# Performance work log

Measured on AMD Instinct MI355X. Metric: run time of the kernel, lower is better.

Reference implementation:

```python
import jax, jax.numpy as jnp
import numpy as np

E4M3_MAX = 448.0
E5M2_MAX = 57344.0

def _q(t, scale, max_rep, dt):
    # divide by scale, saturate to representable range, cast to fp8 (matches torch .to(float8) saturation)
    return jnp.clip(t.astype(jnp.float32) / scale, -max_rep, max_rep).astype(dt)

def setup_inputs() -> dict:
    key = jax.random.key(0)
    k1, k2, k3 = jax.random.split(key, 3)
    B, S, K, N = 4, 2048, 4096, 16384
    x = jax.random.normal(k1, (B, S, K), dtype=jnp.float32).astype(jnp.bfloat16)
    weight = (jax.random.normal(k2, (N, K), dtype=jnp.float32) * 0.02).astype(jnp.bfloat16)
    bias = (jax.random.normal(k3, (N,), dtype=jnp.float32) * 0.01).astype(jnp.bfloat16)
    return {
        "x": x,
        "weight": weight,
        "bias": bias,
        "x_scale": jnp.ones((1,), jnp.float32),   # cold-start unit scales, as in the module
        "w_scale": jnp.ones((1,), jnp.float32),
        "gy_scale": jnp.ones((1,), jnp.float32),
    }

def reference(x, weight, bias, x_scale, w_scale, gy_scale):
    # y = dequant(q_e4m3(x/sx)) @ dequant(q_e4m3(W/sw)).T + b, accumulated in fp32, emitted bf16
    N, K = weight.shape
    leading = x.shape[:-1]
    x_flat = x.reshape(-1, K)                                  # [M, K]
    x_q = _q(x_flat, x_scale, E4M3_MAX, jnp.float8_e4m3fn)     # E4M3 activations
    w_q = _q(weight, w_scale, E4M3_MAX, jnp.float8_e4m3fn)     # E4M3 weights
    x_deq = x_q.astype(jnp.float32) * x_scale                  # cuBLASLt applies scale_a*scale_b in epilogue
    w_deq = w_q.astype(jnp.float32) * w_scale
    y = jnp.einsum('mk,nk->mn', x_deq, w_deq) + bias.astype(jnp.float32)
    return y.astype(jnp.bfloat16).reshape(*leading, N)
```

## Files before the change

### kernel.cpp

```cpp
#include <hip/hip_runtime.h>
#include <hip/hip_bf16.h>
#include <stdint.h>

typedef float f32x4 __attribute__((ext_vector_type(4)));
typedef float f32x16 __attribute__((ext_vector_type(16)));
typedef int i32x4 __attribute__((ext_vector_type(4)));
typedef int i32x8 __attribute__((ext_vector_type(8)));
typedef long i64;

#define BM 256
#define BN 128
#define BKB 64

__device__ __host__ __forceinline__ int swz(int r) {
  return ((r >> 1) ^ (r >> 3)) & 3;
}

__global__ __launch_bounds__(256) void quant_fp8_from_f32(
    const float* __restrict__ in, const float* __restrict__ scale,
    uint8_t* __restrict__ out, int n16) {
  const int i = blockIdx.x * blockDim.x + threadIdx.x;
  if (i >= n16) return;
  const float inv_s = 1.0f / scale[0];
  const float* p = in + (i64)i * 16;
  f32x4 v[4];
  v[0] = *(const f32x4*)p;
  v[1] = *(const f32x4*)(p + 4);
  v[2] = *(const f32x4*)(p + 8);
  v[3] = *(const f32x4*)(p + 12);
  uint32_t w[4];
#pragma unroll
  for (int q = 0; q < 4; q++) {
    float f0 = fminf(fmaxf(v[q][0] * inv_s, -448.f), 448.f);
    float f1 = fminf(fmaxf(v[q][1] * inv_s, -448.f), 448.f);
    float f2 = fminf(fmaxf(v[q][2] * inv_s, -448.f), 448.f);
    float f3 = fminf(fmaxf(v[q][3] * inv_s, -448.f), 448.f);
    int r = 0;
    r = __builtin_amdgcn_cvt_pk_fp8_f32(f0, f1, r, false);
    r = __builtin_amdgcn_cvt_pk_fp8_f32(f2, f3, r, true);
    w[q] = (uint32_t)r;
  }
  ((uint4*)out)[i] = make_uint4(w[0], w[1], w[2], w[3]);
}

__device__ __forceinline__ void gload_lds16(const void* g, void* l) {
  __builtin_amdgcn_global_load_lds(
      (const __attribute__((address_space(1))) uint32_t*)g,
      (__attribute__((address_space(3))) uint32_t*)l, 16, 0, 0);
}

__device__ __forceinline__ float bf16_rne_f32(float f) {
  union { float f; uint32_t u; } c; c.f = f;
  uint32_t lsb = (c.u >> 16) & 1u;
  c.u += 0x7FFFu + lsb;
  c.u &= 0xFFFF0000u;
  return c.f;
}

__global__ __launch_bounds__(256, 2) void gemm_fp8_mx(
    const uint8_t* __restrict__ Aq, const uint8_t* __restrict__ Bq,
    const float* __restrict__ bias,
    const float* __restrict__ xs, const float* __restrict__ wsc,
    float* __restrict__ C, int M, int N, int K) {
  __shared__ uint8_t sA[2][BM * BKB];
  __shared__ uint8_t sB[2][BN * BKB];

  const int nbn = N / BN;
  int bid = blockIdx.x;
  { int cpx = gridDim.x >> 3; bid = (bid & 7) * cpx + (bid >> 3); }
  const int bm = bid / nbn;
  const int bn = bid % nbn;

  const int t = threadIdx.x, lane = t & 63, wave = t >> 6;
  const int wm = (wave >> 1) * 128;
  const int wn = (wave & 1) * 64;
  const int g = lane >> 5;
  const int r31 = lane & 31;

  f32x16 acc[4][2];
#pragma unroll
  for (int i = 0; i < 4; i++)
#pragma unroll
    for (int j = 0; j < 2; j++) acc[i][j] = (f32x16)0.f;

  const int srow = t >> 2;
  const int c16 = t & 3;
  i64 src[4];
#pragma unroll
  for (int j = 0; j < 4; j++) {
    const int row = srow + 64 * j;
    src[j] = (i64)row * K + ((c16 ^ swz(row)) << 4);
  }
  const uint8_t* gA = Aq + (i64)(bm * BM) * K;
  const uint8_t* gB = Bq + (i64)(bn * BN) * K;

  int aoff[4][2], boff[2][2];
#pragma unroll
  for (int i = 0; i < 4; i++) {
    const int ra = wm + i * 32 + r31;
    const int sa_ = swz(ra);
    aoff[i][0] = ra * 64 + (((2 * g + 0) ^ sa_) << 4);
    aoff[i][1] = ra * 64 + (((2 * g + 1) ^ sa_) << 4);
  }
#pragma unroll
  for (int j = 0; j < 2; j++) {
    const int rb = wn + j * 32 + r31;
    const int sb_ = swz(rb);
    boff[j][0] = rb * 64 + (((2 * g + 0) ^ sb_) << 4);
    boff[j][1] = rb * 64 + (((2 * g + 1) ^ sb_) << 4);
  }

  const int NT = K / BKB;
#pragma unroll
  for (int j = 0; j < 4; j++)
    gload_lds16(gA + src[j], &sA[0][t * 16 + j * 4096]);
#pragma unroll
  for (int j = 0; j < 2; j++)
    gload_lds16(gB + src[j], &sB[0][t * 16 + j * 4096]);

  int cur = 0;
  for (int it = 0; it < NT; ++it) {
    if (it + 1 < NT) {
      const i64 kt = (i64)(it + 1) * BKB;
      const int nxt = cur ^ 1;
#pragma unroll
      for (int j = 0; j < 4; j++)
        gload_lds16(gA + src[j] + kt, &sA[nxt][t * 16 + j * 4096]);
#pragma unroll
      for (int j = 0; j < 2; j++)
        gload_lds16(gB + src[j] + kt, &sB[nxt][t * 16 + j * 4096]);
      asm volatile("s_waitcnt vmcnt(6)" ::: "memory");
    } else {
      asm volatile("s_waitcnt vmcnt(0)" ::: "memory");
    }
    __builtin_amdgcn_s_barrier();

    union opnd { i32x4 h[2]; i32x8 v; };
    union opnd ub[2];
#pragma unroll
    for (int j = 0; j < 2; j++) {
      ub[j].h[0] = *(const i32x4*)(&sB[cur][0] + boff[j][0]);
      ub[j].h[1] = *(const i32x4*)(&sB[cur][0] + boff[j][1]);
    }
#pragma unroll
    for (int i = 0; i < 4; i++) {
      union opnd ua;
      ua.h[0] = *(const i32x4*)(&sA[cur][0] + aoff[i][0]);
      ua.h[1] = *(const i32x4*)(&sA[cur][0] + aoff[i][1]);
#pragma unroll
      for (int j = 0; j < 2; j++)
        acc[i][j] = __builtin_amdgcn_mfma_scale_f32_32x32x64_f8f6f4(
            ua.v, ub[j].v, acc[i][j],
            0, 0,
            0, 127,
            0, 127);
    }

    __builtin_amdgcn_s_barrier();
    cur ^= 1;
  }

  const float sc = xs[0] * wsc[0];
#pragma unroll
  for (int j = 0; j < 2; j++) {
    const int col = bn * BN + wn + j * 32 + r31;
    const float bv = bias[col];
#pragma unroll
    for (int i = 0; i < 4; i++) {
      const int rowbase = bm * BM + wm + i * 32 + 4 * g;
#pragma unroll
      for (int reg = 0; reg < 16; reg++) {
        const int row = rowbase + (reg & 3) + 8 * (reg >> 2);
        C[(i64)row * N + col] = bf16_rne_f32(acc[i][j][reg] * sc + bv);
      }
    }
  }
}

extern "C" void kernel_launch(void* const* d_in, const int* in_sizes, int n_in,
                              void* d_out, int out_size, void* d_ws, size_t ws_size,
                              hipStream_t stream) {
  const float* x = (const float*)d_in[0];
  const float* w = (const float*)d_in[1];
  const float* bias = (const float*)d_in[2];
  const float* x_scale = (const float*)d_in[3];
  const float* w_scale = (const float*)d_in[4];

  const int N = in_sizes[2];
  const int K = in_sizes[1] / N;
  const int M = in_sizes[0] / K;

  uint8_t* xq = (uint8_t*)d_ws;
  uint8_t* wq = (uint8_t*)d_ws + (size_t)M * K;

  {
    const int n16 = (M * K) / 16;
    quant_fp8_from_f32<<<(n16 + 255) / 256, 256, 0, stream>>>(x, x_scale, xq, n16);
  }
  {
    const int n16 = (int)(((i64)N * K) / 16);
    quant_fp8_from_f32<<<(n16 + 255) / 256, 256, 0, stream>>>(w, w_scale, wq, n16);
  }

  dim3 grid((M / BM) * (N / BN));
  gemm_fp8_mx<<<grid, 256, 0, stream>>>(
      xq, wq, bias, x_scale, w_scale, (float*)d_out, M, N, K);
}
```

Measured before the change: 723.4 us.

## Load B operand directly from global into registers, bypassing LDS

The weight (B) tile is no longer staged through shared memory. Each wave now loads its own B fragments from global memory straight into registers, one K-step ahead, using ping-pong register buffers, and the loop is unrolled by two to alternate them. The aim is to cut LDS traffic and LDS footprint and to remove the B ds_reads. In exchange, waves that share columns both read the same B data from global memory, the per-row 32-byte accesses coalesce less well, register pressure rises, and the code assumes an even number of K tiles.

```diff
diff --git a/kernel.cpp b/kernel.cpp
--- a/kernel.cpp
+++ b/kernel.cpp
@@ -63,7 +63,6 @@
     const float* __restrict__ xs, const float* __restrict__ wsc,
     float* __restrict__ C, int M, int N, int K) {
   __shared__ uint8_t sA[2][BM * BKB];
-  __shared__ uint8_t sB[2][BN * BKB];
 
   const int nbn = N / BN;
   int bid = blockIdx.x;
@@ -92,9 +91,13 @@
     src[j] = (i64)row * K + ((c16 ^ swz(row)) << 4);
   }
   const uint8_t* gA = Aq + (i64)(bm * BM) * K;
-  const uint8_t* gB = Bq + (i64)(bn * BN) * K;
-
-  int aoff[4][2], boff[2][2];
+
+  const uint8_t* bbase[2];
+#pragma unroll
+  for (int j = 0; j < 2; j++)
+    bbase[j] = Bq + (i64)(bn * BN + wn + j * 32 + r31) * K + g * 32;
+
+  int aoff[4][2];
 #pragma unroll
   for (int i = 0; i < 4; i++) {
     const int ra = wm + i * 32 + r31;
@@ -102,63 +105,56 @@
     aoff[i][0] = ra * 64 + (((2 * g + 0) ^ sa_) << 4);
     aoff[i][1] = ra * 64 + (((2 * g + 1) ^ sa_) << 4);
   }
-#pragma unroll
-  for (int j = 0; j < 2; j++) {
-    const int rb = wn + j * 32 + r31;
-    const int sb_ = swz(rb);
-    boff[j][0] = rb * 64 + (((2 * g + 0) ^ sb_) << 4);
-    boff[j][1] = rb * 64 + (((2 * g + 1) ^ sb_) << 4);
-  }
 
   const int NT = K / BKB;
+  union opnd { i32x4 h[2]; i32x8 v; };
+  opnd ubA[2], ubB[2];
+
 #pragma unroll
   for (int j = 0; j < 4; j++)
     gload_lds16(gA + src[j], &sA[0][t * 16 + j * 4096]);
 #pragma unroll
-  for (int j = 0; j < 2; j++)
-    gload_lds16(gB + src[j], &sB[0][t * 16 + j * 4096]);
-
-  int cur = 0;
-  for (int it = 0; it < NT; ++it) {
-    if (it + 1 < NT) {
-      const i64 kt = (i64)(it + 1) * BKB;
-      const int nxt = cur ^ 1;
-#pragma unroll
-      for (int j = 0; j < 4; j++)
-        gload_lds16(gA + src[j] + kt, &sA[nxt][t * 16 + j * 4096]);
-#pragma unroll
-      for (int j = 0; j < 2; j++)
-        gload_lds16(gB + src[j] + kt, &sB[nxt][t * 16 + j * 4096]);
-      asm volatile("s_waitcnt vmcnt(6)" ::: "memory");
-    } else {
-      asm volatile("s_waitcnt vmcnt(0)" ::: "memory");
-    }
-    __builtin_amdgcn_s_barrier();
-
-    union opnd { i32x4 h[2]; i32x8 v; };
-    union opnd ub[2];
-#pragma unroll
-    for (int j = 0; j < 2; j++) {
-      ub[j].h[0] = *(const i32x4*)(&sB[cur][0] + boff[j][0]);
-      ub[j].h[1] = *(const i32x4*)(&sB[cur][0] + boff[j][1]);
-    }
-#pragma unroll
-    for (int i = 0; i < 4; i++) {
-      union opnd ua;
-      ua.h[0] = *(const i32x4*)(&sA[cur][0] + aoff[i][0]);
-      ua.h[1] = *(const i32x4*)(&sA[cur][0] + aoff[i][1]);
-#pragma unroll
-      for (int j = 0; j < 2; j++)
-        acc[i][j] = __builtin_amdgcn_mfma_scale_f32_32x32x64_f8f6f4(
-            ua.v, ub[j].v, acc[i][j],
-            0, 0,
-            0, 127,
-            0, 127);
-    }
-
-    __builtin_amdgcn_s_barrier();
-    cur ^= 1;
-  }
+  for (int j = 0; j < 2; j++) {
+    ubA[j].h[0] = *(const i32x4*)(bbase[j] + 0);
+    ubA[j].h[1] = *(const i32x4*)(bbase[j] + 16);
+  }
+
+#define STEP(PARITY, UBC, UBN, ITV)                                          \
+  {                                                                          \
+    const int itv = (ITV);                                                   \
+    if (itv + 1 < NT) {                                                      \
+      const i64 kt = (i64)(itv + 1) * BKB;                                   \
+      _Pragma("unroll")                                                      \
+      for (int j = 0; j < 4; j++)                                            \
+        gload_lds16(gA + src[j] + kt, &sA[PARITY ^ 1][t * 16 + j * 4096]);   \
+      _Pragma("unroll")                                                      \
+      for (int j = 0; j < 2; j++) {                                          \
+        UBN[j].h[0] = *(const i32x4*)(bbase[j] + kt);                        \
+        UBN[j].h[1] = *(const i32x4*)(bbase[j] + kt + 16);                   \
+      }                                                                      \
+      asm volatile("s_waitcnt vmcnt(8)" ::: "memory");                       \
+    } else {                                                                 \
+      asm volatile("s_waitcnt vmcnt(0)" ::: "memory");                       \
+    }                                                                        \
+    __builtin_amdgcn_s_barrier();                                            \
+    _Pragma("unroll")                                                        \
+    for (int i = 0; i < 4; i++) {                                            \
+      opnd ua;                                                               \
+      ua.h[0] = *(const i32x4*)(&sA[PARITY][0] + aoff[i][0]);                \
+      ua.h[1] = *(const i32x4*)(&sA[PARITY][0] + aoff[i][1]);                \
+      _Pragma("unroll")                                                      \
+      for (int j = 0; j < 2; j++)                                            \
+        acc[i][j] = __builtin_amdgcn_mfma_scale_f32_32x32x64_f8f6f4(         \
+            ua.v, UBC[j].v, acc[i][j], 0, 0, 0, 127, 0, 127);                \
+    }                                                                        \
+    __builtin_amdgcn_s_barrier();                                            \
+  }
+
+  for (int it = 0; it < NT; it += 2) {
+    STEP(0, ubA, ubB, it);
+    STEP(1, ubB, ubA, it + 1);
+  }
+#undef STEP
 
   const float sc = xs[0] * wsc[0];
 #pragma unroll
```

After: 814.1 us. +12.5%, slower.

## Triple-buffer LDS tiles with prefetch distance two and drop trailing barrier

Applied to the files above, without the earlier changes.

The shared-memory pipeline for the FP8 GEMM goes from two buffers to three. Global-to-LDS loads are now issued two K-tiles ahead, after the B operands for the current tile have been read into registers. With a third buffer, the barrier at the end of each iteration can be removed, since the buffer being overwritten was last read one iteration earlier, before the single remaining barrier. Wave priority is raised around the MFMA block to favour math issue. The cost is 72 KB of LDS per block instead of 48 KB, which tightens occupancy headroom.

```diff
diff --git a/kernel.cpp b/kernel.cpp
--- a/kernel.cpp
+++ b/kernel.cpp
@@ -62,8 +62,8 @@
     const float* __restrict__ bias,
     const float* __restrict__ xs, const float* __restrict__ wsc,
     float* __restrict__ C, int M, int N, int K) {
-  __shared__ uint8_t sA[2][BM * BKB];
-  __shared__ uint8_t sB[2][BN * BKB];
+  __shared__ uint8_t sA[3][BM * BKB];
+  __shared__ uint8_t sB[3][BN * BKB];
 
   const int nbn = N / BN;
   int bid = blockIdx.x;
@@ -112,41 +112,55 @@
 
   const int NT = K / BKB;
 #pragma unroll
-  for (int j = 0; j < 4; j++)
+  for (int j = 0; j < 4; j++) {
     gload_lds16(gA + src[j], &sA[0][t * 16 + j * 4096]);
+  }
 #pragma unroll
   for (int j = 0; j < 2; j++)
     gload_lds16(gB + src[j], &sB[0][t * 16 + j * 4096]);
-
-  int cur = 0;
+#pragma unroll
+  for (int j = 0; j < 4; j++)
+    gload_lds16(gA + src[j] + BKB, &sA[1][t * 16 + j * 4096]);
+#pragma unroll
+  for (int j = 0; j < 2; j++)
+    gload_lds16(gB + src[j] + BKB, &sB[1][t * 16 + j * 4096]);
+
+  int cur = 0, st2 = 2;
   for (int it = 0; it < NT; ++it) {
     if (it + 1 < NT) {
-      const i64 kt = (i64)(it + 1) * BKB;
-      const int nxt = cur ^ 1;
-#pragma unroll
-      for (int j = 0; j < 4; j++)
-        gload_lds16(gA + src[j] + kt, &sA[nxt][t * 16 + j * 4096]);
-#pragma unroll
-      for (int j = 0; j < 2; j++)
-        gload_lds16(gB + src[j] + kt, &sB[nxt][t * 16 + j * 4096]);
       asm volatile("s_waitcnt vmcnt(6)" ::: "memory");
     } else {
       asm volatile("s_waitcnt vmcnt(0)" ::: "memory");
     }
     __builtin_amdgcn_s_barrier();
 
+    const uint8_t* bufA = &sA[cur][0];
+    const uint8_t* bufB = &sB[cur][0];
+
     union opnd { i32x4 h[2]; i32x8 v; };
-    union opnd ub[2];
+    opnd ub[2];
 #pragma unroll
     for (int j = 0; j < 2; j++) {
-      ub[j].h[0] = *(const i32x4*)(&sB[cur][0] + boff[j][0]);
-      ub[j].h[1] = *(const i32x4*)(&sB[cur][0] + boff[j][1]);
-    }
+      ub[j].h[0] = *(const i32x4*)(bufB + boff[j][0]);
+      ub[j].h[1] = *(const i32x4*)(bufB + boff[j][1]);
+    }
+
+    if (it + 2 < NT) {
+      const i64 kt = (i64)(it + 2) * BKB;
+#pragma unroll
+      for (int j = 0; j < 4; j++)
+        gload_lds16(gA + src[j] + kt, &sA[st2][t * 16 + j * 4096]);
+#pragma unroll
+      for (int j = 0; j < 2; j++)
+        gload_lds16(gB + src[j] + kt, &sB[st2][t * 16 + j * 4096]);
+    }
+
+    __builtin_amdgcn_s_setprio(1);
 #pragma unroll
     for (int i = 0; i < 4; i++) {
-      union opnd ua;
-      ua.h[0] = *(const i32x4*)(&sA[cur][0] + aoff[i][0]);
-      ua.h[1] = *(const i32x4*)(&sA[cur][0] + aoff[i][1]);
+      opnd ua;
+      ua.h[0] = *(const i32x4*)(bufA + aoff[i][0]);
+      ua.h[1] = *(const i32x4*)(bufA + aoff[i][1]);
 #pragma unroll
       for (int j = 0; j < 2; j++)
         acc[i][j] = __builtin_amdgcn_mfma_scale_f32_32x32x64_f8f6f4(
@@ -155,9 +169,10 @@
             0, 127,
             0, 127);
     }
-
-    __builtin_amdgcn_s_barrier();
-    cur ^= 1;
+    __builtin_amdgcn_s_setprio(0);
+
+    cur = (cur == 2) ? 0 : cur + 1;
+    st2 = (st2 == 2) ? 0 : st2 + 1;
   }
 
   const float sc = xs[0] * wsc[0];
```

Measured after the change: 725.7 us. About the same (+0.3%).
